# Kernel tuning notes

Measured on AMD Instinct MI355X. Metric: run time of the kernel, lower is better.

The kernel has to match this reference:

```python
import jax, jax.numpy as jnp
import numpy as np

NUM_USER = 20000
NUM_ITEM = 40000
N_NODES = NUM_USER + NUM_ITEM
DIM = 64
V_DIM = 2048
T_DIM = 768
N_EDGES = 1_000_000
K_USER = 40
K_ITEM = 10
N_LAYERS = 2


def setup_inputs() -> dict:
    key = jax.random.key(0)
    ks = iter(jax.random.split(key, 32))

    def xavier(shape):
        s = (2.0 / (shape[0] + shape[-1])) ** 0.5
        return jax.random.normal(next(ks), shape, jnp.float32) * s

    # bipartite user-item interactions, doubled (undirected), as in DRAGON.__init__
    u = jax.random.randint(next(ks), (N_EDGES,), 0, NUM_USER)
    it = jax.random.randint(next(ks), (N_EDGES,), NUM_USER, N_NODES)
    edge_index = jnp.stack([jnp.concatenate([u, it]), jnp.concatenate([it, u])])

    v_feat = jax.random.normal(next(ks), (NUM_ITEM, V_DIM), jnp.float32)
    t_feat = jax.random.normal(next(ks), (NUM_ITEM, T_DIM), jnp.float32)

    # KNN item-item adjacency (top-10 per row) with symmetric-normalized values,
    # mirroring get_knn_adj_mat/compute_normalized_laplacian
    rows = jnp.repeat(jnp.arange(NUM_ITEM), K_ITEM)
    cols = jax.random.randint(next(ks), (NUM_ITEM * K_ITEM,), 0, NUM_ITEM)
    mm_indices = jnp.stack([rows, cols])
    row_sum = jax.ops.segment_sum(jnp.ones(NUM_ITEM * K_ITEM, jnp.float32), rows,
                                  num_segments=NUM_ITEM) + 1e-7
    rinv = row_sum ** -0.5
    mm_values = rinv[rows] * rinv[cols]

    user_graph = jax.random.randint(next(ks), (NUM_USER, K_USER), 0, NUM_USER)
    user_weight_matrix = jax.nn.softmax(
        jax.random.normal(next(ks), (NUM_USER, K_USER), jnp.float32), axis=1)
    weight_u = jax.nn.softmax(
        jax.random.normal(next(ks), (NUM_USER, 2, 1), jnp.float32), axis=1)

    return {
        'edge_index': edge_index,
        'v_feat': v_feat, 't_feat': t_feat,
        'v_pref': xavier((NUM_USER, DIM)), 't_pref': xavier((NUM_USER, DIM)),
        'v_mlp1_w': xavier((V_DIM, 4 * DIM)), 'v_mlp1_b': jnp.zeros(4 * DIM, jnp.float32),
        'v_mlp2_w': xavier((4 * DIM, DIM)), 'v_mlp2_b': jnp.zeros(DIM, jnp.float32),
        't_mlp1_w': xavier((T_DIM, 4 * DIM)), 't_mlp1_b': jnp.zeros(4 * DIM, jnp.float32),
        't_mlp2_w': xavier((4 * DIM, DIM)), 't_mlp2_b': jnp.zeros(DIM, jnp.float32),
        'v_conv_w': xavier((DIM, DIM)), 'v_conv_b': jnp.zeros(DIM, jnp.float32),
        't_conv_w': xavier((DIM, DIM)), 't_conv_b': jnp.zeros(DIM, jnp.float32),
        'weight_u': weight_u,
        'user_graph': user_graph,
        'user_weight_matrix': user_weight_matrix,
        'mm_indices': mm_indices,
        'mm_values': mm_values,
    }


def _l2n(x):
    n = jnp.linalg.norm(x, axis=-1, keepdims=True)
    return x / jnp.maximum(n, 1e-12)


def reference(edge_index, v_feat, t_feat, v_pref, t_pref,
              v_mlp1_w, v_mlp1_b, v_mlp2_w, v_mlp2_b,
              t_mlp1_w, t_mlp1_b, t_mlp2_w, t_mlp2_b,
              v_conv_w, v_conv_b, t_conv_w, t_conv_b,
              weight_u, user_graph, user_weight_matrix,
              mm_indices, mm_values):
    seg = jax.ops.segment_sum
    # GCNConv normalization with self-loops (shared by both branches)
    sl = jnp.arange(N_NODES)
    src = jnp.concatenate([edge_index[0], sl])
    dst = jnp.concatenate([edge_index[1], sl])
    deg = seg(jnp.ones_like(dst, dtype=jnp.float32), dst, num_segments=N_NODES)
    dinv = deg ** -0.5
    norm = (dinv[src] * dinv[dst])[:, None]

    def conv(x, w, b):  # out[dst] += norm * (x @ w)[src], then bias
        return seg(norm * (x @ w)[src], dst, num_segments=N_NODES) + b

    def branch(feat, pref, w1, b1, w2, b2, cw, cb):
        temp = jax.nn.leaky_relu(feat @ w1 + b1) @ w2 + b2  # [I, D]
        x = _l2n(jnp.concatenate([pref, temp], axis=0))      # [N, D]
        h = conv(x, cw, cb)
        h1 = conv(h, cw, cb)
        return x + h + h1

    v_rep = branch(v_feat, v_pref, v_mlp1_w, v_mlp1_b, v_mlp2_w, v_mlp2_b, v_conv_w, v_conv_b)
    t_rep = branch(t_feat, t_pref, t_mlp1_w, t_mlp1_b, t_mlp2_w, t_mlp2_b, t_conv_w, t_conv_b)

    representation = jnp.concatenate([v_rep, t_rep], axis=1)  # [N, 2D]
    wu = weight_u[:, :, 0]  # [U, 2]
    user_rep = jnp.concatenate([wu[:, 0:1] * v_rep[:NUM_USER],
                                wu[:, 1:2] * t_rep[:NUM_USER]], axis=1)  # [U, 2D]
    item_rep = representation[NUM_USER:]  # [I, 2D]

    # User_Graph_sample: weighted sum over sampled user neighborhoods
    h_u = jnp.einsum('uk,ukd->ud', user_weight_matrix, user_rep[user_graph])
    user_rep = user_rep + h_u

    # n_layers of sparse Laplacian propagation over KNN item-item graph
    row, col = mm_indices[0], mm_indices[1]
    h_i = item_rep
    for _ in range(N_LAYERS):
        h_i = seg(mm_values[:, None] * h_i[col], row, num_segments=NUM_ITEM)
    item_rep = item_rep + h_i

    return jnp.concatenate([user_rep, item_rep], axis=0)  # [N, 2D]
```

## Files before the change

### kernel.cpp

```cpp
#include <hip/hip_runtime.h>

#define NUSER 20000
#define NITEM 40000
#define NNODE 60000
#define DIM   64
#define NE    1000000
#define KUSER 40
#define KITEM 10

typedef __attribute__((ext_vector_type(8))) short short8v;
typedef __attribute__((ext_vector_type(4))) float floatx4;

__device__ inline short bf16rne(float f) {
    unsigned u = __builtin_bit_cast(unsigned, f);
    unsigned r = (u + 0x7fffu + ((u >> 16) & 1u)) >> 16;
    return (short)r;
}
__device__ inline unsigned cvt_pk_bf16(float lo, float hi) {
    unsigned r;
    asm("v_cvt_pk_bf16_f32 %0, %1, %2" : "=v"(r) : "v"(lo), "v"(hi));
    return r;
}
__device__ inline float bflo(unsigned v) { return __builtin_bit_cast(float, v << 16); }
__device__ inline float bfhi(unsigned v) { return __builtin_bit_cast(float, v & 0xffff0000u); }

__global__ __launch_bounds__(256) void k_count(const int* __restrict__ dst, int* __restrict__ cnt, int n) {
    int i = blockIdx.x * 256 + threadIdx.x;
    if (i < n) atomicAdd(&cnt[dst[i]], 1);
}

__global__ __launch_bounds__(256) void k_dinv(const int* __restrict__ cnt, float* __restrict__ dinv) {
    int i = blockIdx.x * 256 + threadIdx.x;
    if (i < NNODE) dinv[i] = 1.0f / sqrtf((float)(cnt[i] + 1));
}

__global__ __launch_bounds__(256) void k_scanA(const int* __restrict__ v, int* __restrict__ excl,
                                               int* __restrict__ bsum, int n) {
    __shared__ int s[256];
    int t = threadIdx.x, i = blockIdx.x * 256 + t;
    int orig = (i < n) ? v[i] : 0;
    s[t] = orig; __syncthreads();
    #pragma unroll
    for (int off = 1; off < 256; off <<= 1) {
        int u = (t >= off) ? s[t - off] : 0;
        __syncthreads();
        s[t] += u;
        __syncthreads();
    }
    if (i < n) excl[i] = s[t] - orig;
    if (t == 255) bsum[blockIdx.x] = s[255];
}

__global__ __launch_bounds__(256) void k_scanB(int* __restrict__ bsum, int nb) {
    __shared__ int s[256];
    int t = threadIdx.x;
    int orig = (t < nb) ? bsum[t] : 0;
    s[t] = orig; __syncthreads();
    #pragma unroll
    for (int off = 1; off < 256; off <<= 1) {
        int u = (t >= off) ? s[t - off] : 0;
        __syncthreads();
        s[t] += u;
        __syncthreads();
    }
    if (t < nb) bsum[t] = s[t] - orig;
}

__global__ __launch_bounds__(256) void k_scanC(int* __restrict__ excl, const int* __restrict__ bsum,
                                               int* __restrict__ cursor, int n) {
    int i = blockIdx.x * 256 + threadIdx.x;
    if (i < n) {
        int v = excl[i] + bsum[blockIdx.x];
        excl[i] = v;
        cursor[i] = v;
    }
    if (i == 0) excl[n] = 2 * NE;
}

__global__ __launch_bounds__(256) void k_fill(const int* __restrict__ src, const int* __restrict__ dst,
                                              const float* __restrict__ dinv, int* __restrict__ cursor,
                                              unsigned* __restrict__ csr_pkd, int n) {
    int i = blockIdx.x * 256 + threadIdx.x;
    if (i >= n) return;
    int s = src[i], d = dst[i];
    unsigned pk = ((unsigned)(unsigned short)bf16rne(dinv[s]) << 16) | (unsigned)s;
    int pos = atomicAdd(&cursor[d], 1);
    csr_pkd[pos] = pk;
}

__global__ __launch_bounds__(256) void k_transpose_bf16(const float* __restrict__ B, short* __restrict__ Btb,
                                                        int K, int N) {
    __shared__ float s[16][17];
    int t = threadIdx.x, tx = t & 15, ty = t >> 4;
    int k0 = blockIdx.x * 16, n0 = blockIdx.y * 16;
    s[ty][tx] = B[(size_t)(k0 + ty) * N + n0 + tx];
    __syncthreads();
    int k = k0 + tx, n = n0 + ty;
    Btb[(size_t)(k >> 5) * (N * 32) + n * 32 + (k & 31)] = bf16rne(s[tx][ty]);
}

__global__ __launch_bounds__(256) void k_prep(const float* __restrict__ Wv, const float* __restrict__ Wt,
                                              const float* __restrict__ bv, const float* __restrict__ bt,
                                              short* __restrict__ Bcat, float* __restrict__ bw, float* __restrict__ bb) {
    __shared__ float Wld[2][64][65];
    __shared__ float W2ld[2][64][65];
    int t = threadIdx.x;
    for (int id = t; id < 8192; id += 256) {
        int z = id >> 12, k = (id >> 6) & 63, n = id & 63;
        Wld[z][k][n] = (z ? Wt : Wv)[k * 64 + n];
    }
    __syncthreads();
    for (int id = t; id < 8192; id += 256) {
        int z = id >> 12, k = (id >> 6) & 63, n = id & 63;
        float a = 0.f;
        #pragma unroll 8
        for (int m = 0; m < 64; m++) a += Wld[z][k][m] * Wld[z][m][n];
        W2ld[z][k][n] = a;
    }
    __syncthreads();
    for (int id = t; id < 32768; id += 256) {
        int k = id >> 7, n = id & 127;
        int kb = k >> 6, kk = k & 63;
        float v = 0.f;
        if (kb == 0)      { if (n < 64)  v = Wld[0][kk][n]; }
        else if (kb == 1) { if (n >= 64) v = Wld[1][kk][n - 64]; }
        else if (kb == 2) { if (n < 64)  v = W2ld[0][kk][n]; }
        else              { if (n >= 64) v = W2ld[1][kk][n - 64]; }
        Bcat[(k >> 5) * 4096 + n * 32 + (k & 31)] = bf16rne(v);
    }
    if (t < 128) {
        int z = t >> 6, n = t & 63;
        const float* b = z ? bt : bv;
        float a = 0.f;
        #pragma unroll 8
        for (int k = 0; k < 64; k++) a += b[k] * Wld[z][k][n];
        bw[t] = a;
        bb[t] = 2.f * b[n];
    }
}

#define AP   40
#define MIDP 264
__global__ __launch_bounds__(256) void mlp_fused(const float* __restrict__ A, const short* __restrict__ B1t,
                                                 const float* __restrict__ b1, const short* __restrict__ B2t,
                                                 const float* __restrict__ b2,
                                                 unsigned* __restrict__ xbf, int boff, int K) {
    __shared__ short smem[64 * MIDP];
    short* As = smem;
    const int tid = threadIdx.x;
    const int lane = tid & 63, wid = tid >> 6;
    const int rowBase = blockIdx.x * 64;

    const int sar = tid >> 2, sac = (tid & 3) * 8;
    const float* aptr = A + (size_t)(rowBase + sar) * K + sac;

    const int fk = (lane >> 4) * 8;
    const int faoff = (lane & 15) * AP + fk;
    const int bcol0 = wid * 64 + (lane & 15);

    floatx4 acc[4][4];
    #pragma unroll
    for (int m = 0; m < 4; m++)
        #pragma unroll
        for (int n = 0; n < 4; n++) acc[m][n] = (floatx4)0.f;

    float4 ra0, ra1;
    const int nk = K >> 5;

    auto ldg = [&](int ks) {
        const float* ap = aptr + ks * 32;
        ra0 = *(const float4*)(ap);
        ra1 = *(const float4*)(ap + 4);
    };
    auto stv = [&](int buf) {
        uint4 av;
        av.x = cvt_pk_bf16(ra0.x, ra0.y); av.y = cvt_pk_bf16(ra0.z, ra0.w);
        av.z = cvt_pk_bf16(ra1.x, ra1.y); av.w = cvt_pk_bf16(ra1.z, ra1.w);
        *(uint4*)&As[buf * (64 * AP) + sar * AP + sac] = av;
    };

    ldg(0); stv(0);
    __syncthreads();
    int cur = 0;
    for (int ks = 0; ks < nk; ++ks) {
        if (ks + 1 < nk) ldg(ks + 1);
        short8v a[4], b[4];
        #pragma unroll
        for (int n = 0; n < 4; n++)
            b[n] = *(const short8v*)(B1t + (size_t)ks * 8192 + (bcol0 + n * 16) * 32 + fk);
        #pragma unroll
        for (int m = 0; m < 4; m++) a[m] = *(const short8v*)&As[cur * (64 * AP) + faoff + m * 16 * AP];
        #pragma unroll
        for (int m = 0; m < 4; m++)
            #pragma unroll
            for (int n = 0; n < 4; n++)
                acc[m][n] = __builtin_amdgcn_mfma_f32_16x16x32_bf16(a[m], b[n], acc[m][n], 0, 0, 0);
        if (ks + 1 < nk) stv(cur ^ 1);
        __syncthreads();
        cur ^= 1;
    }

    short* mid = smem;
    float bcol[4];
    #pragma unroll
    for (int n = 0; n < 4; n++) bcol[n] = b1[wid * 64 + n * 16 + (lane & 15)];
    #pragma unroll
    for (int m = 0; m < 4; m++)
        #pragma unroll
        for (int n = 0; n < 4; n++)
            #pragma unroll
            for (int q = 0; q < 4; q++) {
                int row = m * 16 + (lane >> 4) * 4 + q;
                int col = wid * 64 + n * 16 + (lane & 15);
                float v = acc[m][n][q] + bcol[n];
                v = v > 0.f ? v : 0.01f * v;
                mid[row * MIDP + col] = bf16rne(v);
            }
    __syncthreads();

    floatx4 acc2[4];
    #pragma unroll
    for (int n2 = 0; n2 < 4; n2++) acc2[n2] = (floatx4)0.f;
    const int arow = wid * 16 + (lane & 15);
    #pragma unroll
    for (int ks2 = 0; ks2 < 8; ++ks2) {
        short8v af = *(const short8v*)&mid[arow * MIDP + ks2 * 32 + fk];
        const short* bp = B2t + ks2 * 2048 + fk;
        short8v bf4[4];
        #pragma unroll
        for (int n2 = 0; n2 < 4; n2++) bf4[n2] = *(const short8v*)(bp + (n2 * 16 + (lane & 15)) * 32);
        #pragma unroll
        for (int n2 = 0; n2 < 4; n2++)
            acc2[n2] = __builtin_amdgcn_mfma_f32_16x16x32_bf16(af, bf4[n2], acc2[n2], 0, 0, 0);
    }

    float b2c[4];
    #pragma unroll
    for (int n2 = 0; n2 < 4; n2++) b2c[n2] = b2[n2 * 16 + (lane & 15)];
    #pragma unroll
    for (int q = 0; q < 4; ++q) {
        float v[4]; float ss = 0.f;
        #pragma unroll
        for (int n2 = 0; n2 < 4; n2++) { v[n2] = acc2[n2][q] + b2c[n2]; ss += v[n2] * v[n2]; }
        ss += __shfl_xor(ss, 1, 64);
        ss += __shfl_xor(ss, 2, 64);
        ss += __shfl_xor(ss, 4, 64);
        ss += __shfl_xor(ss, 8, 64);
        float sc = 1.f / fmaxf(sqrtf(ss), 1e-12f);
        int grow = rowBase + wid * 16 + (lane >> 4) * 4 + q;
        #pragma unroll
        for (int n2 = 0; n2 < 4; n2++) {
            float xn = v[n2] * sc;
            float pn = __shfl_xor(xn, 1, 64);
            if (!(lane & 1))
                xbf[(size_t)grow * 64 + boff + n2 * 8 + ((lane & 15) >> 1)] = cvt_pk_bf16(xn, pn);
        }
    }
}

__global__ __launch_bounds__(256) void k_l2n_pref(const float* __restrict__ prefv, const float* __restrict__ preft,
                                                  unsigned* __restrict__ xbf) {
    int row = blockIdx.x * 4 + (threadIdx.x >> 6);
    int lane = threadIdx.x & 63;
    if (row >= NUSER) return;
    const float* p = blockIdx.y ? preft : prefv;
    float v = p[(size_t)row * 64 + lane];
    float ss = v * v;
    #pragma unroll
    for (int off = 32; off >= 1; off >>= 1) ss += __shfl_xor(ss, off, 64);
    float xn = v / fmaxf(sqrtf(ss), 1e-12f);
    float pn = __shfl_xor(xn, 1, 64);
    if (!(lane & 1))
        xbf[(size_t)row * 64 + (blockIdx.y ? 32 : 0) + (lane >> 1)] = cvt_pk_bf16(xn, pn);
}

__global__ __launch_bounds__(256) void k_gather_p(const int* __restrict__ rowptr, const unsigned* __restrict__ csr_pkd,
                                                  const float* __restrict__ dinv, const unsigned* __restrict__ in_bf,
                                                  unsigned* __restrict__ out_bf, float* __restrict__ s_out) {
    int row = blockIdx.x * 4 + (threadIdx.x >> 6);
    int lane = threadIdx.x & 63;
    if (row >= NNODE) return;
    int p0 = rowptr[row], p1 = rowptr[row + 1];
    float dr = dinv[row];
    unsigned sv = in_bf[(size_t)row * 64 + lane];
    float ax0 = dr * bflo(sv), ay0 = dr * bfhi(sv);
    float ax1 = 0.f, ay1 = 0.f;
    float wsum = 0.f;
    for (int p = p0; p < p1; p += 64) {
        int c = p1 - p; if (c > 64) c = 64;
        unsigned pk = (lane < c) ? csr_pkd[p + lane] : 0u;
        wsum += bfhi(pk);
        int j = 0;
        for (; j + 4 <= c; j += 4) {
            unsigned e0 = __shfl(pk, j, 64),     e1 = __shfl(pk, j + 1, 64);
            unsigned e2 = __shfl(pk, j + 2, 64), e3 = __shfl(pk, j + 3, 64);
            unsigned v0 = in_bf[(size_t)(e0 & 0xffffu) * 64 + lane];
            unsigned v1 = in_bf[(size_t)(e1 & 0xffffu) * 64 + lane];
            unsigned v2 = in_bf[(size_t)(e2 & 0xffffu) * 64 + lane];
            unsigned v3 = in_bf[(size_t)(e3 & 0xffffu) * 64 + lane];
            float w0 = bfhi(e0), w1 = bfhi(e1), w2 = bfhi(e2), w3 = bfhi(e3);
            ax0 += w0 * bflo(v0); ay0 += w0 * bfhi(v0);
            ax1 += w1 * bflo(v1); ay1 += w1 * bfhi(v1);
            ax0 += w2 * bflo(v2); ay0 += w2 * bfhi(v2);
            ax1 += w3 * bflo(v3); ay1 += w3 * bfhi(v3);
        }
        for (; j < c; ++j) {
            unsigned e = __shfl(pk, j, 64);
            unsigned v = in_bf[(size_t)(e & 0xffffu) * 64 + lane];
            float w = bfhi(e);
            ax0 += w * bflo(v); ay0 += w * bfhi(v);
        }
    }
    out_bf[(size_t)row * 64 + lane] = cvt_pk_bf16(dr * (ax0 + ax1), dr * (ay0 + ay1));
    #pragma unroll
    for (int o = 32; o >= 1; o >>= 1) wsum += __shfl_xor(wsum, o, 64);
    if (lane == 0) s_out[row] = dr * (dr + wsum);
}

__global__ __launch_bounds__(512) void k_gather2_rep(const int* __restrict__ rowptr, const unsigned* __restrict__ csr_pkd,
                                                     const float* __restrict__ dinv, const unsigned* __restrict__ g1,
                                                     const short* __restrict__ Bcat, const unsigned* __restrict__ x_bf,
                                                     const float* __restrict__ s, const float* __restrict__ bw,
                                                     const float* __restrict__ bb, const float* __restrict__ weight_u,
                                                     float* __restrict__ rep0, unsigned* __restrict__ rep_bf) {
    __shared__ short As[16 * 264];
    const int tid = threadIdx.x, lane = tid & 63, w = tid >> 6;
    const int rowBase = blockIdx.x * 16;

    for (int rr = 0; rr < 2; ++rr) {
        int lrow = w * 2 + rr;
        int row = rowBase + lrow;
        int p0 = rowptr[row], p1 = rowptr[row + 1];
        float dr = dinv[row];
        unsigned sv = g1[(size_t)row * 64 + lane];
        float ax0 = dr * bflo(sv), ay0 = dr * bfhi(sv);
        float ax1 = 0.f, ay1 = 0.f;
        for (int p = p0; p < p1; p += 64) {
            int c = p1 - p; if (c > 64) c = 64;
            unsigned pk = (lane < c) ? csr_pkd[p + lane] : 0u;
            int j = 0;
            for (; j + 4 <= c; j += 4) {
                unsigned e0 = __shfl(pk, j, 64),     e1 = __shfl(pk, j + 1, 64);
                unsigned e2 = __shfl(pk, j + 2, 64), e3 = __shfl(pk, j + 3, 64);
                unsigned v0 = g1[(size_t)(e0 & 0xffffu) * 64 + lane];
                unsigned v1 = g1[(size_t)(e1 & 0xffffu) * 64 + lane];
                unsigned v2 = g1[(size_t)(e2 & 0xffffu) * 64 + lane];
                unsigned v3 = g1[(size_t)(e3 & 0xffffu) * 64 + lane];
                float w0 = bfhi(e0), w1 = bfhi(e1), w2 = bfhi(e2), w3 = bfhi(e3);
                ax0 += w0 * bflo(v0); ay0 += w0 * bfhi(v0);
                ax1 += w1 * bflo(v1); ay1 += w1 * bfhi(v1);
                ax0 += w2 * bflo(v2); ay0 += w2 * bfhi(v2);
                ax1 += w3 * bflo(v3); ay1 += w3 * bfhi(v3);
            }
            for (; j < c; ++j) {
                unsigned e = __shfl(pk, j, 64);
                unsigned v = g1[(size_t)(e & 0xffffu) * 64 + lane];
                float wj = bfhi(e);
                ax0 += wj * bflo(v); ay0 += wj * bfhi(v);
            }
        }
        *(unsigned*)&As[lrow * 264 + 2 * lane] = sv;
        *(unsigned*)&As[lrow * 264 + 128 + 2 * lane] = cvt_pk_bf16(dr * (ax0 + ax1), dr * (ay0 + ay1));
    }
    __syncthreads();

    const int fk = (lane >> 4) * 8;
    floatx4 acc = (floatx4)0.f;
    #pragma unroll
    for (int ks = 0; ks < 8; ++ks) {
        short8v af = *(const short8v*)&As[(lane & 15) * 264 + ks * 32 + fk];
        short8v bf = *(const short8v*)(Bcat + ks * 4096 + (w * 16 + (lane & 15)) * 32 + fk);
        acc = __builtin_amdgcn_mfma_f32_16x16x32_bf16(af, bf, acc, 0, 0, 0);
    }
    const int col = w * 16 + (lane & 15);
    const float bwc = bw[col], bbc = bb[col];
    #pragma unroll
    for (int q = 0; q < 4; ++q) {
        int lrow = (lane >> 4) * 4 + q;
        int row = rowBase + lrow;
        unsigned xw = x_bf[(size_t)row * 64 + (col >> 1)];
        float xval = (col & 1) ? bfhi(xw) : bflo(xw);
        float v = acc[q] + xval + s[row] * bwc + bbc;
        float wu = (row < NUSER) ? weight_u[row * 2 + (col >> 6)] : 1.0f;
        v *= wu;
        rep0[(size_t)row * 128 + col] = v;
        float pn = __shfl_xor(v, 1, 64);
        if (!(lane & 1))
            rep_bf[(size_t)row * 64 + (col >> 1)] = cvt_pk_bf16(v, pn);
    }
}

#define UBLK (NUSER * 64 / 256)
__global__ __launch_bounds__(256) void k_user_item1(const float* __restrict__ rep0, const unsigned* __restrict__ rep_bf,
                                                    const int* __restrict__ ug, const float* __restrict__ uwm,
                                                    const int* __restrict__ mm_col, const float* __restrict__ mm_values,
                                                    float* __restrict__ out, unsigned* __restrict__ tmp_bf) {
    int bid = blockIdx.x;
    if (bid < UBLK) {
        int id = bid * 256 + threadIdx.x;
        int u = id >> 6, lane = id & 63;
        float2 acc = *(const float2*)(rep0 + (size_t)u * 128 + 2 * lane);
        #pragma unroll 4
        for (int k = 0; k < KUSER; k++) {
            int nb = ug[u * KUSER + k];
            float w = uwm[u * KUSER + k];
            unsigned v = rep_bf[(size_t)nb * 64 + lane];
            acc.x += w * bflo(v);
            acc.y += w * bfhi(v);
        }
        *(float2*)(out + (size_t)u * 128 + 2 * lane) = acc;
    } else {
        int id = (bid - UBLK) * 256 + threadIdx.x;
        int r = id >> 6, lane = id & 63;
        float ax = 0.f, ay = 0.f;
        #pragma unroll
        for (int j = 0; j < KITEM; j++) {
            int c = mm_col[r * KITEM + j];
            float w = mm_values[r * KITEM + j];
            unsigned v = rep_bf[(size_t)(NUSER + c) * 64 + lane];
            ax += w * bflo(v);
            ay += w * bfhi(v);
        }
        tmp_bf[(size_t)r * 64 + lane] = cvt_pk_bf16(ax, ay);
    }
}

__global__ __launch_bounds__(256) void k_item2(const float* __restrict__ rep0, const unsigned* __restrict__ tmp_bf,
                                               const int* __restrict__ mm_col, const float* __restrict__ mm_values,
                                               float* __restrict__ out) {
    int id = blockIdx.x * 256 + threadIdx.x;
    int r = id >> 6, lane = id & 63;
    if (r >= NITEM) return;
    float ax = 0.f, ay = 0.f;
    #pragma unroll
    for (int j = 0; j < KITEM; j++) {
        int c = mm_col[r * KITEM + j];
        float w = mm_values[r * KITEM + j];
        unsigned v = tmp_bf[(size_t)c * 64 + lane];
        ax += w * bflo(v);
        ay += w * bfhi(v);
    }
    float2 base = *(const float2*)(rep0 + (size_t)(NUSER + r) * 128 + 2 * lane);
    float2 o;
    o.x = base.x + ax;
    o.y = base.y + ay;
    *(float2*)(out + (size_t)(NUSER + r) * 128 + 2 * lane) = o;
}

extern "C" void kernel_launch(void* const* d_in, const int* in_sizes, int n_in,
                              void* d_out, int out_size, void* d_ws, size_t ws_size,
                              hipStream_t stream) {
    const int*   edge_index = (const int*)d_in[0];
    const float* v_feat   = (const float*)d_in[1];
    const float* t_feat   = (const float*)d_in[2];
    const float* v_pref   = (const float*)d_in[3];
    const float* t_pref   = (const float*)d_in[4];
    const float* v_mlp1_w = (const float*)d_in[5];
    const float* v_mlp1_b = (const float*)d_in[6];
    const float* v_mlp2_w = (const float*)d_in[7];
    const float* v_mlp2_b = (const float*)d_in[8];
    const float* t_mlp1_w = (const float*)d_in[9];
    const float* t_mlp1_b = (const float*)d_in[10];
    const float* t_mlp2_w = (const float*)d_in[11];
    const float* t_mlp2_b = (const float*)d_in[12];
    const float* v_conv_w = (const float*)d_in[13];
    const float* v_conv_b = (const float*)d_in[14];
    const float* t_conv_w = (const float*)d_in[15];
    const float* t_conv_b = (const float*)d_in[16];
    const float* weight_u = (const float*)d_in[17];
    const int*   user_graph = (const int*)d_in[18];
    const float* uwm      = (const float*)d_in[19];
    const int*   mm_indices = (const int*)d_in[20];
    const float* mm_values  = (const float*)d_in[21];
    float* out = (float*)d_out;

    char* wsb = (char*)d_ws;
    size_t off = 0;
    auto alloc = [&](size_t bytes) -> void* {
        void* p = wsb + off;
        off = (off + bytes + 255) & ~(size_t)255;
        return p;
    };
    int*      cnt     = (int*)     alloc(NNODE * 4);
    float*    dinv    = (float*)   alloc(NNODE * 4);
    int*      rowptr  = (int*)     alloc((NNODE + 1) * 4);
    int*      bsum    = (int*)     alloc(256 * 4);
    int*      cursor  = (int*)     alloc(NNODE * 4);
    unsigned* csr_pkd = (unsigned*)alloc((size_t)2 * NE * 4);
    short*    Btw     = (short*)   alloc((size_t)2048 * 256 * 2);
    short*    W2b     = (short*)   alloc((size_t)256 * 64 * 2);
    short*    Bcat    = (short*)   alloc((size_t)256 * 128 * 2);
    float*    bw      = (float*)   alloc(128 * 4);
    float*    bb      = (float*)   alloc(128 * 4);
    float*    svec    = (float*)   alloc(NNODE * 4);
    unsigned* x_bf    = (unsigned*)alloc((size_t)NNODE * 64 * 4);
    unsigned* g1      = (unsigned*)alloc((size_t)NNODE * 64 * 4);
    float*    rep0    = (float*)   alloc((size_t)NNODE * 128 * 4);
    unsigned* rep_bf  = (unsigned*)alloc((size_t)NNODE * 64 * 4);
    unsigned* tmp_bf  = (unsigned*)alloc((size_t)NITEM * 64 * 4);
    (void)ws_size; (void)n_in; (void)in_sizes; (void)out_size;

    const int* e_src = edge_index;
    const int* e_dst = edge_index + 2 * NE;
    const int* mm_col = mm_indices + NITEM * KITEM;

    const int NB = (NNODE + 255) / 256;

    hipMemsetAsync(cnt, 0, NNODE * 4, stream);
    k_count<<<(2 * NE + 255) / 256, 256, 0, stream>>>(e_dst, cnt, 2 * NE);
    k_dinv<<<(NNODE + 255) / 256, 256, 0, stream>>>(cnt, dinv);
    k_scanA<<<NB, 256, 0, stream>>>(cnt, rowptr, bsum, NNODE);
    k_scanB<<<1, 256, 0, stream>>>(bsum, NB);
    k_scanC<<<NB, 256, 0, stream>>>(rowptr, bsum, cursor, NNODE);
    k_fill<<<(2 * NE + 255) / 256, 256, 0, stream>>>(e_src, e_dst, dinv, cursor, csr_pkd, 2 * NE);

    k_prep<<<1, 256, 0, stream>>>(v_conv_w, t_conv_w, v_conv_b, t_conv_b, Bcat, bw, bb);

    {
        dim3 t1(2048 / 16, 16);
        k_transpose_bf16<<<t1, 256, 0, stream>>>(v_mlp1_w, Btw, 2048, 256);
        dim3 t2(256 / 16, 4);
        k_transpose_bf16<<<t2, 256, 0, stream>>>(v_mlp2_w, W2b, 256, 64);
        mlp_fused<<<NITEM / 64, 256, 0, stream>>>(v_feat, Btw, v_mlp1_b, W2b, v_mlp2_b,
                                                  x_bf + (size_t)NUSER * 64, 0, 2048);
        dim3 t3(768 / 16, 16);
        k_transpose_bf16<<<t3, 256, 0, stream>>>(t_mlp1_w, Btw, 768, 256);
        k_transpose_bf16<<<t2, 256, 0, stream>>>(t_mlp2_w, W2b, 256, 64);
        mlp_fused<<<NITEM / 64, 256, 0, stream>>>(t_feat, Btw, t_mlp1_b, W2b, t_mlp2_b,
                                                  x_bf + (size_t)NUSER * 64, 32, 768);
    }
    {
        dim3 g(NUSER / 4, 2);
        k_l2n_pref<<<g, 256, 0, stream>>>(v_pref, t_pref, x_bf);
    }

    k_gather_p<<<(NNODE + 3) / 4, 256, 0, stream>>>(rowptr, csr_pkd, dinv, x_bf, g1, svec);
    k_gather2_rep<<<NNODE / 16, 512, 0, stream>>>(rowptr, csr_pkd, dinv, g1, Bcat, x_bf,
                                                  svec, bw, bb, weight_u, rep0, rep_bf);

    k_user_item1<<<UBLK + NITEM * 64 / 256, 256, 0, stream>>>(rep0, rep_bf, user_graph, uwm,
                                                              mm_col, mm_values, out, tmp_bf);
    k_item2<<<NITEM * 64 / 256, 256, 0, stream>>>(rep0, tmp_bf, mm_col, mm_values, out);
}
```

Measured before the change: 617.4 us.

## Merge setup kernels, batch weight transposes, and stage MLP B tiles in LDS

Several small preprocessing kernels are merged. Edge counting and CSR fill now process each undirected pair once, and the dinv computation is folded into the scan. The four weight transposes run as one launch, and the v/t MLP kernels become a single merged launch, so the text branch can run concurrently with the visual one. The MLP also double-buffers the B1 tile through LDS instead of reading it from global memory per wave, at the cost of more shared memory per block and possibly lower occupancy.

Result: faster. 582.4 us (-5.7%).

```diff
diff --git a/kernel.cpp b/kernel.cpp
--- a/kernel.cpp
+++ b/kernel.cpp
@@ -24,21 +24,20 @@
 __device__ inline float bflo(unsigned v) { return __builtin_bit_cast(float, v << 16); }
 __device__ inline float bfhi(unsigned v) { return __builtin_bit_cast(float, v & 0xffff0000u); }
 
-__global__ __launch_bounds__(256) void k_count(const int* __restrict__ dst, int* __restrict__ cnt, int n) {
+__global__ __launch_bounds__(256) void k_count_pair(const int* __restrict__ uu, const int* __restrict__ it,
+                                                    int* __restrict__ cnt) {
     int i = blockIdx.x * 256 + threadIdx.x;
-    if (i < n) atomicAdd(&cnt[dst[i]], 1);
-}
-
-__global__ __launch_bounds__(256) void k_dinv(const int* __restrict__ cnt, float* __restrict__ dinv) {
-    int i = blockIdx.x * 256 + threadIdx.x;
-    if (i < NNODE) dinv[i] = 1.0f / sqrtf((float)(cnt[i] + 1));
+    if (i >= NE) return;
+    atomicAdd(&cnt[uu[i]], 1);
+    atomicAdd(&cnt[it[i]], 1);
 }
 
 __global__ __launch_bounds__(256) void k_scanA(const int* __restrict__ v, int* __restrict__ excl,
-                                               int* __restrict__ bsum, int n) {
+                                               int* __restrict__ bsum, float* __restrict__ dinv, int n) {
     __shared__ int s[256];
     int t = threadIdx.x, i = blockIdx.x * 256 + t;
     int orig = (i < n) ? v[i] : 0;
+    if (i < n) dinv[i] = 1.0f / sqrtf((float)(orig + 1));
     s[t] = orig; __syncthreads();
     #pragma unroll
     for (int off = 1; off < 256; off <<= 1) {
@@ -77,26 +76,38 @@
     if (i == 0) excl[n] = 2 * NE;
 }
 
-__global__ __launch_bounds__(256) void k_fill(const int* __restrict__ src, const int* __restrict__ dst,
-                                              const float* __restrict__ dinv, int* __restrict__ cursor,
-                                              unsigned* __restrict__ csr_pkd, int n) {
+__global__ __launch_bounds__(256) void k_fill_pair(const int* __restrict__ uu, const int* __restrict__ it,
+                                                   const float* __restrict__ dinv, int* __restrict__ cursor,
+                                                   unsigned* __restrict__ csr_pkd) {
     int i = blockIdx.x * 256 + threadIdx.x;
-    if (i >= n) return;
-    int s = src[i], d = dst[i];
-    unsigned pk = ((unsigned)(unsigned short)bf16rne(dinv[s]) << 16) | (unsigned)s;
-    int pos = atomicAdd(&cursor[d], 1);
-    csr_pkd[pos] = pk;
-}
-
-__global__ __launch_bounds__(256) void k_transpose_bf16(const float* __restrict__ B, short* __restrict__ Btb,
-                                                        int K, int N) {
+    if (i >= NE) return;
+    int u = uu[i], t = it[i];
+    unsigned pku = ((unsigned)(unsigned short)bf16rne(dinv[u]) << 16) | (unsigned)u;
+    unsigned pkt = ((unsigned)(unsigned short)bf16rne(dinv[t]) << 16) | (unsigned)t;
+    int pos1 = atomicAdd(&cursor[t], 1);
+    csr_pkd[pos1] = pku;
+    int pos2 = atomicAdd(&cursor[u], 1);
+    csr_pkd[pos2] = pkt;
+}
+
+__global__ __launch_bounds__(256) void k_transpose_all(const float* __restrict__ W1v, const float* __restrict__ W1t,
+                                                       const float* __restrict__ W2v, const float* __restrict__ W2t,
+                                                       short* __restrict__ Bv, short* __restrict__ Bt,
+                                                       short* __restrict__ B2v, short* __restrict__ B2t) {
     __shared__ float s[16][17];
+    int bid = blockIdx.x;
+    const float* B; short* D; int K, N, local;
+    if (bid < 2048)      { B = W1v; D = Bv;  K = 2048; N = 256; local = bid; }
+    else if (bid < 2816) { B = W1t; D = Bt;  K = 768;  N = 256; local = bid - 2048; }
+    else if (bid < 2880) { B = W2v; D = B2v; K = 256;  N = 64;  local = bid - 2816; }
+    else                 { B = W2t; D = B2t; K = 256;  N = 64;  local = bid - 2880; }
+    int ktiles = K >> 4;
+    int k0 = (local % ktiles) * 16, n0 = (local / ktiles) * 16;
     int t = threadIdx.x, tx = t & 15, ty = t >> 4;
-    int k0 = blockIdx.x * 16, n0 = blockIdx.y * 16;
     s[ty][tx] = B[(size_t)(k0 + ty) * N + n0 + tx];
     __syncthreads();
     int k = k0 + tx, n = n0 + ty;
-    Btb[(size_t)(k >> 5) * (N * 32) + n * 32 + (k & 31)] = bf16rne(s[tx][ty]);
+    D[(size_t)(k >> 5) * (N * 32) + n * 32 + (k & 31)] = bf16rne(s[tx][ty]);
 }
 
 __global__ __launch_bounds__(256) void k_prep(const float* __restrict__ Wv, const float* __restrict__ Wt,
@@ -141,22 +152,34 @@
 
 #define AP   40
 #define MIDP 264
-__global__ __launch_bounds__(256) void mlp_fused(const float* __restrict__ A, const short* __restrict__ B1t,
-                                                 const float* __restrict__ b1, const short* __restrict__ B2t,
-                                                 const float* __restrict__ b2,
-                                                 unsigned* __restrict__ xbf, int boff, int K) {
-    __shared__ short smem[64 * MIDP];
+#define VBLKS (NITEM / 64)
+__global__ __launch_bounds__(256) void mlp_merged(const float* __restrict__ Av, const float* __restrict__ At,
+                                                  const short* __restrict__ B1v, const short* __restrict__ B1t,
+                                                  const float* __restrict__ b1v, const float* __restrict__ b1t,
+                                                  const short* __restrict__ B2v, const short* __restrict__ B2t,
+                                                  const float* __restrict__ b2v, const float* __restrict__ b2t,
+                                                  unsigned* __restrict__ xbf) {
+    __shared__ short smem[2 * 64 * AP + 2 * 256 * AP];
     short* As = smem;
+    short* Bs = smem + 2 * 64 * AP;
+    const bool isV = blockIdx.x < VBLKS;
+    const float* A    = isV ? Av : At;
+    const short* B1t_ = isV ? B1v : B1t;
+    const float* b1   = isV ? b1v : b1t;
+    const short* B2t_ = isV ? B2v : B2t;
+    const float* b2   = isV ? b2v : b2t;
+    const int K = isV ? 2048 : 768;
+    const int boff = isV ? 0 : 32;
+    const int rowBase = (isV ? blockIdx.x : blockIdx.x - VBLKS) * 64;
+
     const int tid = threadIdx.x;
     const int lane = tid & 63, wid = tid >> 6;
-    const int rowBase = blockIdx.x * 64;
-
     const int sar = tid >> 2, sac = (tid & 3) * 8;
     const float* aptr = A + (size_t)(rowBase + sar) * K + sac;
 
     const int fk = (lane >> 4) * 8;
     const int faoff = (lane & 15) * AP + fk;
-    const int bcol0 = wid * 64 + (lane & 15);
+    const int fboff = (wid * 64 + (lane & 15)) * AP + fk;
 
     floatx4 acc[4][4];
     #pragma unroll
@@ -165,18 +188,25 @@
         for (int n = 0; n < 4; n++) acc[m][n] = (floatx4)0.f;
 
     float4 ra0, ra1;
+    short8v rb[4];
     const int nk = K >> 5;
 
     auto ldg = [&](int ks) {
         const float* ap = aptr + ks * 32;
         ra0 = *(const float4*)(ap);
         ra1 = *(const float4*)(ap + 4);
+        const short* bsrc = B1t_ + (size_t)ks * 8192 + tid * 8;
+        #pragma unroll
+        for (int it = 0; it < 4; it++) rb[it] = *(const short8v*)(bsrc + it * 2048);
     };
     auto stv = [&](int buf) {
         uint4 av;
         av.x = cvt_pk_bf16(ra0.x, ra0.y); av.y = cvt_pk_bf16(ra0.z, ra0.w);
         av.z = cvt_pk_bf16(ra1.x, ra1.y); av.w = cvt_pk_bf16(ra1.z, ra1.w);
         *(uint4*)&As[buf * (64 * AP) + sar * AP + sac] = av;
+        #pragma unroll
+        for (int it = 0; it < 4; it++)
+            *(short8v*)&Bs[buf * (256 * AP) + (sar + it * 64) * AP + sac] = rb[it];
     };
 
     ldg(0); stv(0);
@@ -186,10 +216,9 @@
         if (ks + 1 < nk) ldg(ks + 1);
         short8v a[4], b[4];
         #pragma unroll
-        for (int n = 0; n < 4; n++)
-            b[n] = *(const short8v*)(B1t + (size_t)ks * 8192 + (bcol0 + n * 16) * 32 + fk);
-        #pragma unroll
         for (int m = 0; m < 4; m++) a[m] = *(const short8v*)&As[cur * (64 * AP) + faoff + m * 16 * AP];
+        #pragma unroll
+        for (int n = 0; n < 4; n++) b[n] = *(const short8v*)&Bs[cur * (256 * AP) + fboff + n * 16 * AP];
         #pragma unroll
         for (int m = 0; m < 4; m++)
             #pragma unroll
@@ -200,7 +229,7 @@
         cur ^= 1;
     }
 
-    short* mid = smem;
+    short* mid = Bs;
     float bcol[4];
     #pragma unroll
     for (int n = 0; n < 4; n++) bcol[n] = b1[wid * 64 + n * 16 + (lane & 15)];
@@ -225,7 +254,7 @@
     #pragma unroll
     for (int ks2 = 0; ks2 < 8; ++ks2) {
         short8v af = *(const short8v*)&mid[arow * MIDP + ks2 * 32 + fk];
-        const short* bp = B2t + ks2 * 2048 + fk;
+        const short* bp = B2t_ + ks2 * 2048 + fk;
         short8v bf4[4];
         #pragma unroll
         for (int n2 = 0; n2 < 4; n2++) bf4[n2] = *(const short8v*)(bp + (n2 * 16 + (lane & 15)) * 32);
@@ -247,7 +276,7 @@
         ss += __shfl_xor(ss, 4, 64);
         ss += __shfl_xor(ss, 8, 64);
         float sc = 1.f / fmaxf(sqrtf(ss), 1e-12f);
-        int grow = rowBase + wid * 16 + (lane >> 4) * 4 + q;
+        int grow = NUSER + rowBase + wid * 16 + (lane >> 4) * 4 + q;
         #pragma unroll
         for (int n2 = 0; n2 < 4; n2++) {
             float xn = v[n2] * sc;
@@ -487,8 +516,10 @@
     int*      bsum    = (int*)     alloc(256 * 4);
     int*      cursor  = (int*)     alloc(NNODE * 4);
     unsigned* csr_pkd = (unsigned*)alloc((size_t)2 * NE * 4);
-    short*    Btw     = (short*)   alloc((size_t)2048 * 256 * 2);
-    short*    W2b     = (short*)   alloc((size_t)256 * 64 * 2);
+    short*    Btw_v   = (short*)   alloc((size_t)2048 * 256 * 2);
+    short*    Btw_t   = (short*)   alloc((size_t)768 * 256 * 2);
+    short*    W2b_v   = (short*)   alloc((size_t)256 * 64 * 2);
+    short*    W2b_t   = (short*)   alloc((size_t)256 * 64 * 2);
     short*    Bcat    = (short*)   alloc((size_t)256 * 128 * 2);
     float*    bw      = (float*)   alloc(128 * 4);
     float*    bb      = (float*)   alloc(128 * 4);
@@ -500,35 +531,25 @@
     unsigned* tmp_bf  = (unsigned*)alloc((size_t)NITEM * 64 * 4);
     (void)ws_size; (void)n_in; (void)in_sizes; (void)out_size;
 
-    const int* e_src = edge_index;
-    const int* e_dst = edge_index + 2 * NE;
+    const int* pairs_u  = edge_index;
+    const int* pairs_it = edge_index + NE;
     const int* mm_col = mm_indices + NITEM * KITEM;
 
     const int NB = (NNODE + 255) / 256;
 
     hipMemsetAsync(cnt, 0, NNODE * 4, stream);
-    k_count<<<(2 * NE + 255) / 256, 256, 0, stream>>>(e_dst, cnt, 2 * NE);
-    k_dinv<<<(NNODE + 255) / 256, 256, 0, stream>>>(cnt, dinv);
-    k_scanA<<<NB, 256, 0, stream>>>(cnt, rowptr, bsum, NNODE);
+    k_count_pair<<<(NE + 255) / 256, 256, 0, stream>>>(pairs_u, pairs_it, cnt);
+    k_scanA<<<NB, 256, 0, stream>>>(cnt, rowptr, bsum, dinv, NNODE);
     k_scanB<<<1, 256, 0, stream>>>(bsum, NB);
     k_scanC<<<NB, 256, 0, stream>>>(rowptr, bsum, cursor, NNODE);
-    k_fill<<<(2 * NE + 255) / 256, 256, 0, stream>>>(e_src, e_dst, dinv, cursor, csr_pkd, 2 * NE);
+    k_fill_pair<<<(NE + 255) / 256, 256, 0, stream>>>(pairs_u, pairs_it, dinv, cursor, csr_pkd);
 
     k_prep<<<1, 256, 0, stream>>>(v_conv_w, t_conv_w, v_conv_b, t_conv_b, Bcat, bw, bb);
-
-    {
-        dim3 t1(2048 / 16, 16);
-        k_transpose_bf16<<<t1, 256, 0, stream>>>(v_mlp1_w, Btw, 2048, 256);
-        dim3 t2(256 / 16, 4);
-        k_transpose_bf16<<<t2, 256, 0, stream>>>(v_mlp2_w, W2b, 256, 64);
-        mlp_fused<<<NITEM / 64, 256, 0, stream>>>(v_feat, Btw, v_mlp1_b, W2b, v_mlp2_b,
-                                                  x_bf + (size_t)NUSER * 64, 0, 2048);
-        dim3 t3(768 / 16, 16);
-        k_transpose_bf16<<<t3, 256, 0, stream>>>(t_mlp1_w, Btw, 768, 256);
-        k_transpose_bf16<<<t2, 256, 0, stream>>>(t_mlp2_w, W2b, 256, 64);
-        mlp_fused<<<NITEM / 64, 256, 0, stream>>>(t_feat, Btw, t_mlp1_b, W2b, t_mlp2_b,
-                                                  x_bf + (size_t)NUSER * 64, 32, 768);
-    }
+    k_transpose_all<<<2944, 256, 0, stream>>>(v_mlp1_w, t_mlp1_w, v_mlp2_w, t_mlp2_w,
+                                              Btw_v, Btw_t, W2b_v, W2b_t);
+
+    mlp_merged<<<2 * VBLKS, 256, 0, stream>>>(v_feat, t_feat, Btw_v, Btw_t, v_mlp1_b, t_mlp1_b,
+                                              W2b_v, W2b_t, v_mlp2_b, t_mlp2_b, x_bf);
     {
         dim3 g(NUSER / 4, 2);
         k_l2n_pref<<<g, 256, 0, stream>>>(v_pref, t_pref, x_bf);
```
